# Performance work log

Measured on AMD Instinct MI355X. Metric: run time of the kernel, lower is better.

## Reference

```python
import jax, jax.numpy as jnp
import numpy as np

B, T, D = 4, 2048, 1024
H, KD, VD = 16, 64, 64  # num_heads, key_dim, value_dim; H*KD == D


def setup_inputs() -> dict:
    key = jax.random.key(0)
    ks = jax.random.split(key, 10)
    s = 0.02
    return {
        "q_in": jax.random.normal(ks[0], (B, T, D), jnp.float32),
        "v_in": jax.random.normal(ks[1], (B, T, D), jnp.float32),
        "Wq": jax.random.normal(ks[2], (D, H * KD), jnp.float32) * s,
        "bq": jnp.zeros((H * KD,), jnp.float32),
        "Wk": jax.random.normal(ks[3], (D, H * KD), jnp.float32) * s,
        "bk": jnp.zeros((H * KD,), jnp.float32),
        "Wv": jax.random.normal(ks[4], (D, H * VD), jnp.float32) * s,
        "bv": jnp.zeros((H * VD,), jnp.float32),
        "Wo": jax.random.normal(ks[5], (H * VD, D), jnp.float32) * s,
        "bo": jnp.zeros((D,), jnp.float32),
    }


def reference(q_in, v_in, Wq, bq, Wk, bk, Wv, bv, Wo, bo):
    # QKV projections (key defaults to value input)
    q = q_in @ Wq + bq                      # [B,T,H*KD]
    k = v_in @ Wk + bk                      # [B,T,H*KD]
    v = v_in @ Wv + bv                      # [B,T,H*VD]
    q = q.reshape(B, T, H, KD)
    k = k.reshape(B, T, H, KD)
    v = v.reshape(B, T, H, VD)
    # scaled dot-product attention, scores materialized as [B,H,Tq,Tv]
    q = q / jnp.sqrt(jnp.asarray(KD, q.dtype))
    scores = jnp.einsum('bqnh,bvnh->bnqv', q, k)
    weights = jax.nn.softmax(scores, axis=-1)
    out = jnp.einsum('bnqv,bvnh->bqnh', weights, v)  # [B,Tq,H,VD]
    out = out.reshape(B, T, H * VD)
    return out @ Wo + bo                    # [B,T,D]
```

## Files before the change

kernel.cpp:

```cpp
#include <hip/hip_runtime.h>

#define BATCH  4
#define T_SEQ  2048
#define NH     16
#define DMODEL 1024
#define HD     64

typedef float    f32x4 __attribute__((ext_vector_type(4)));
typedef _Float16 f16x8 __attribute__((ext_vector_type(8)));
typedef _Float16 f16x4 __attribute__((ext_vector_type(4)));
typedef __fp16   h16x2 __attribute__((ext_vector_type(2)));

#define LOG2E 1.44269504088896f

__device__ __forceinline__ void lds_load16(const void* g, void* l) {
  __builtin_amdgcn_global_load_lds((const __attribute__((address_space(1))) void*)g,
                                   (__attribute__((address_space(3))) void*)l, 16, 0, 0);
}

__device__ __forceinline__ f16x4 pack4_f16(float a, float b, float c, float d) {
  union { h16x2 h[2]; f16x4 f; } u;
  u.h[0] = __builtin_amdgcn_cvt_pkrtz(a, b);
  u.h[1] = __builtin_amdgcn_cvt_pkrtz(c, d);
  return u.f;
}

__global__ __launch_bounds__(256) void cast2_f32_to_f16(
    const float* __restrict__ a, const float* __restrict__ bsrc,
    _Float16* __restrict__ oa, _Float16* __restrict__ ob, int n4) {
  const float* in = blockIdx.y ? bsrc : a;
  _Float16* out = blockIdx.y ? ob : oa;
  int i = blockIdx.x * 256 + threadIdx.x;
  if (i < n4) {
    float4 v = ((const float4*)in)[i];
    f16x4 o = { (_Float16)v.x, (_Float16)v.y, (_Float16)v.z, (_Float16)v.w };
    ((f16x4*)out)[i] = o;
  }
}

__global__ __launch_bounds__(256) void transcast_w4(
    const float* __restrict__ W0, const float* __restrict__ W1,
    const float* __restrict__ W2, const float* __restrict__ W3,
    _Float16* __restrict__ T0, _Float16* __restrict__ T1,
    _Float16* __restrict__ T2, _Float16* __restrict__ T3) {
  const float* W; _Float16* Wt;
  switch (blockIdx.z) {
    case 0: W = W0; Wt = T0; break;
    case 1: W = W1; Wt = T1; break;
    case 2: W = W2; Wt = T2; break;
    default: W = W3; Wt = T3; break;
  }
  __shared__ float L[64][65];
  const int n0 = blockIdx.x * 64, k0 = blockIdx.y * 64;
  const int tx = threadIdx.x & 15, ty = threadIdx.x >> 4;
#pragma unroll
  for (int i = 0; i < 4; ++i) {
    float4 v = *(const float4*)&W[(size_t)(k0 + ty + 16 * i) * DMODEL + n0 + tx * 4];
    L[ty + 16 * i][tx * 4 + 0] = v.x;
    L[ty + 16 * i][tx * 4 + 1] = v.y;
    L[ty + 16 * i][tx * 4 + 2] = v.z;
    L[ty + 16 * i][tx * 4 + 3] = v.w;
  }
  __syncthreads();
#pragma unroll
  for (int i = 0; i < 4; ++i) {
    int n = n0 + ty + 16 * i;
    f16x4 o;
#pragma unroll
    for (int j = 0; j < 4; ++j) o[j] = (_Float16)L[tx * 4 + j][ty + 16 * i];
    *(f16x4*)&Wt[(size_t)n * DMODEL + k0 + tx * 4] = o;
  }
}

__device__ __forceinline__ void gemm2_body(
    const _Float16* __restrict__ A, const _Float16* __restrict__ Wt,
    const float* __restrict__ bias, void* __restrict__ Cout, float scale,
    int mode, _Float16* As0, _Float16* As1, _Float16* Bs0, _Float16* Bs1) {
  const int K = DMODEL;
  const int lane = threadIdx.x & 63, wave = threadIdx.x >> 6;
  const int bid = blockIdx.x + blockIdx.y * gridDim.x;
  const int m0 = ((bid & 7) * 4 + ((bid >> 3) & 3)) * 256;
  const int n0 = (bid >> 5) * 128;
  const int wm4 = (wave & 3) * 4;
  const int wn4 = (wave >> 2) * 4;
  const int m16 = lane & 15, quad = lane >> 4;

  const _Float16* ap[4]; const _Float16* bp[2];
#pragma unroll
  for (int j = 0; j < 4; ++j) {
    int g = wave * 4 + j;
    ap[j] = A + (size_t)(m0 + (g >> 1) * 16 + m16) * K + (g & 1) * 32 + quad * 8;
  }
#pragma unroll
  for (int j = 0; j < 2; ++j) {
    int g = wave * 2 + j;
    bp[j] = Wt + (size_t)(n0 + (g >> 1) * 16 + m16) * K + (g & 1) * 32 + quad * 8;
  }

  f32x4 acc[4][4] = {};

  _Float16 *Ac = As0, *An = As1, *Bc = Bs0, *Bn = Bs1;

#pragma unroll
  for (int j = 0; j < 4; ++j) lds_load16(ap[j], Ac + (wave * 4 + j) * 512);
#pragma unroll
  for (int j = 0; j < 2; ++j) lds_load16(bp[j], Bc + (wave * 2 + j) * 512);
  __syncthreads();

  for (int kt = 0; kt < 16; ++kt) {
    if (kt < 15) {
      const int k0 = (kt + 1) * 64;
#pragma unroll
      for (int j = 0; j < 4; ++j) lds_load16(ap[j] + k0, An + (wave * 4 + j) * 512);
#pragma unroll
      for (int j = 0; j < 2; ++j) lds_load16(bp[j] + k0, Bn + (wave * 2 + j) * 512);
    }
#pragma unroll
    for (int s = 0; s < 2; ++s) {
      f16x8 bf[4];
#pragma unroll
      for (int t = 0; t < 4; ++t)
        bf[t] = *(const f16x8*)(Bc + (((wn4 + t) * 2 + s) * 64 + lane) * 8);
#pragma unroll
      for (int mi = 0; mi < 4; ++mi) {
        f16x8 af = *(const f16x8*)(Ac + (((wm4 + mi) * 2 + s) * 64 + lane) * 8);
#pragma unroll
        for (int ni = 0; ni < 4; ++ni)
          acc[mi][ni] = __builtin_amdgcn_mfma_f32_16x16x32_f16(af, bf[ni], acc[mi][ni], 0, 0, 0);
      }
    }
    __syncthreads();
    _Float16* tA = Ac; Ac = An; An = tA;
    _Float16* tB = Bc; Bc = Bn; Bn = tB;
  }

  if (mode == 2) {
#pragma unroll
    for (int mi = 0; mi < 4; ++mi)
#pragma unroll
      for (int ni = 0; ni < 4; ++ni) {
        int row = m0 + (wm4 + mi) * 16 + quad * 4;
        int col = n0 + (wn4 + ni) * 16 + m16;
        int bb = row >> 11, tt = row & (T_SEQ - 1);
        int hh = col >> 6, dd = col & 63;
        float bv = bias[col];
        f16x4 pv = pack4_f16(acc[mi][ni][0] + bv, acc[mi][ni][1] + bv,
                             acc[mi][ni][2] + bv, acc[mi][ni][3] + bv);
        *(f16x4*)&((_Float16*)Cout)[(((size_t)bb * NH + hh) * HD + dd) * T_SEQ + tt] = pv;
      }
  } else if (mode == 0) {
#pragma unroll
    for (int mi = 0; mi < 4; ++mi)
#pragma unroll
      for (int r = 0; r < 4; ++r) {
        int row = m0 + (wm4 + mi) * 16 + quad * 4 + r;
#pragma unroll
        for (int ni = 0; ni < 4; ++ni) {
          int col = n0 + (wn4 + ni) * 16 + m16;
          float v = (acc[mi][ni][r] + bias[col]) * scale;
          ((_Float16*)Cout)[(size_t)row * DMODEL + col] = (_Float16)v;
        }
      }
  } else {
#pragma unroll
    for (int mi = 0; mi < 4; ++mi)
#pragma unroll
      for (int r = 0; r < 4; ++r) {
        int row = m0 + (wm4 + mi) * 16 + quad * 4 + r;
#pragma unroll
        for (int ni = 0; ni < 4; ++ni) {
          int col = n0 + (wn4 + ni) * 16 + m16;
          ((float*)Cout)[(size_t)row * DMODEL + col] = acc[mi][ni][r] + bias[col];
        }
      }
  }
}

__global__ __launch_bounds__(512, 2) void gemm_qkv(
    const _Float16* __restrict__ Aq, const _Float16* __restrict__ Av,
    const _Float16* __restrict__ Wq, const _Float16* __restrict__ Wk,
    const _Float16* __restrict__ Wv,
    const float* __restrict__ bq, const float* __restrict__ bk,
    const float* __restrict__ bv,
    _Float16* __restrict__ Cq, _Float16* __restrict__ Ck, _Float16* __restrict__ Cv) {
  __shared__ _Float16 As[2][256 * 64];
  __shared__ _Float16 Bs[2][128 * 64];
  const _Float16* A; const _Float16* Wt; const float* bias; _Float16* C;
  float scale; int mode;
  if (blockIdx.z == 0)      { A = Aq; Wt = Wq; bias = bq; C = Cq; scale = 0.125f * LOG2E; mode = 0; }
  else if (blockIdx.z == 1) { A = Av; Wt = Wk; bias = bk; C = Ck; scale = 1.f; mode = 0; }
  else                      { A = Av; Wt = Wv; bias = bv; C = Cv; scale = 1.f; mode = 2; }
  gemm2_body(A, Wt, bias, C, scale, mode, As[0], As[1], Bs[0], Bs[1]);
}

__global__ __launch_bounds__(512, 2) void gemm_out(
    const _Float16* __restrict__ A, const _Float16* __restrict__ Wt,
    const float* __restrict__ bias, float* __restrict__ Cout) {
  __shared__ _Float16 As[2][256 * 64];
  __shared__ _Float16 Bs[2][128 * 64];
  gemm2_body(A, Wt, bias, Cout, 1.f, 3, As[0], As[1], Bs[0], Bs[1]);
}

__global__ __launch_bounds__(256, 2) void attn_mfma(
    const _Float16* __restrict__ Q, const _Float16* __restrict__ Kb,
    const _Float16* __restrict__ Vt, _Float16* __restrict__ O) {
  __shared__ _Float16 Ks[64 * 64], Vs[64 * 64];
  __shared__ _Float16 Ps[4 * 4096];

  const int lane = threadIdx.x & 63, wave = threadIdx.x >> 6;
  const int m16 = lane & 15, quad = lane >> 4;
  const int h = blockIdx.x;
  const int q0 = blockIdx.y * 256;
  const int b = blockIdx.z;
  const int wq = wave * 64;
  const int wbase = wave * 4096;

  f16x8 qf[4][2];
#pragma unroll
  for (int mi = 0; mi < 4; ++mi)
#pragma unroll
    for (int ki = 0; ki < 2; ++ki) {
      int q = q0 + wq + mi * 16 + m16;
      qf[mi][ki] = *(const f16x8*)(Q + (((size_t)b * T_SEQ + q) * NH + h) * HD + ki * 32 + quad * 8);
    }

  const _Float16 *kp[2], *vp[2];
#pragma unroll
  for (int i = 0; i < 2; ++i) {
    int g = wave * 128 + i * 64 + lane;
    int tk = (g >> 7) * 16 + (g & 15);
    int dkof = ((g >> 6) & 1) * 32 + ((g >> 4) & 3) * 8;
    kp[i] = Kb + (((size_t)b * T_SEQ + tk) * NH + h) * HD + dkof;
    int dvof = (g >> 7) * 16 + (g & 15);
    int tv = ((g >> 6) & 1) * 32 + ((g >> 4) & 3) * 8;
    vp[i] = Vt + (((size_t)b * NH + h) * HD + dvof) * T_SEQ + tv;
  }

  int pw[4][4];
#pragma unroll
  for (int mi = 0; mi < 4; ++mi)
#pragma unroll
    for (int nt = 0; nt < 4; ++nt) {
      int kt = nt >> 1;
      int q8 = ((nt & 1) << 1) | (quad >> 1);
      pw[mi][nt] = wbase + ((mi * 2 + kt) * 64 + q8 * 16 + m16) * 8 + (quad & 1) * 4;
    }

  const f16x8 onef = {(_Float16)1, (_Float16)1, (_Float16)1, (_Float16)1,
                      (_Float16)1, (_Float16)1, (_Float16)1, (_Float16)1};

  f32x4 o_acc[4][4] = {};
  f32x4 l_acc[4] = {};

  for (int kv = 0; kv < T_SEQ; kv += 64) {
    __syncthreads();
#pragma unroll
    for (int i = 0; i < 2; ++i) {
      lds_load16(kp[i] + (size_t)kv * (NH * HD), Ks + (wave * 2 + i) * 512);
      lds_load16(vp[i] + kv, Vs + (wave * 2 + i) * 512);
    }
    __syncthreads();

    f32x4 st[4][4] = {};
#pragma unroll
    for (int nt = 0; nt < 4; ++nt)
#pragma unroll
      for (int ki = 0; ki < 2; ++ki) {
        f16x8 kf = *(const f16x8*)(Ks + ((nt * 2 + ki) * 64 + lane) * 8);
#pragma unroll
        for (int mi = 0; mi < 4; ++mi)
          st[mi][nt] = __builtin_amdgcn_mfma_f32_16x16x32_f16(kf, qf[mi][ki], st[mi][nt], 0, 0, 0);
      }

#pragma unroll
    for (int mi = 0; mi < 4; ++mi)
#pragma unroll
      for (int nt = 0; nt < 4; ++nt) {
        f16x4 p = pack4_f16(__builtin_amdgcn_exp2f(st[mi][nt][0]),
                            __builtin_amdgcn_exp2f(st[mi][nt][1]),
                            __builtin_amdgcn_exp2f(st[mi][nt][2]),
                            __builtin_amdgcn_exp2f(st[mi][nt][3]));
        *(f16x4*)(Ps + pw[mi][nt]) = p;
      }

#pragma unroll
    for (int kt = 0; kt < 2; ++kt) {
      f16x8 pf[4];
#pragma unroll
      for (int mi = 0; mi < 4; ++mi) {
        pf[mi] = *(const f16x8*)(Ps + wbase + ((mi * 2 + kt) * 64 + lane) * 8);
        l_acc[mi] = __builtin_amdgcn_mfma_f32_16x16x32_f16(pf[mi], onef, l_acc[mi], 0, 0, 0);
      }
#pragma unroll
      for (int nd = 0; nd < 4; ++nd) {
        f16x8 vf = *(const f16x8*)(Vs + ((nd * 2 + kt) * 64 + lane) * 8);
#pragma unroll
        for (int mi = 0; mi < 4; ++mi)
          o_acc[mi][nd] = __builtin_amdgcn_mfma_f32_16x16x32_f16(pf[mi], vf, o_acc[mi][nd], 0, 0, 0);
      }
    }
  }

#pragma unroll
  for (int mi = 0; mi < 4; ++mi)
#pragma unroll
    for (int r = 0; r < 4; ++r) {
      float inv = 1.f / l_acc[mi][r];
      int q = q0 + wq + mi * 16 + quad * 4 + r;
#pragma unroll
      for (int nd = 0; nd < 4; ++nd) {
        int d = nd * 16 + m16;
        O[(((size_t)b * T_SEQ + q) * NH + h) * HD + d] = (_Float16)(o_acc[mi][nd][r] * inv);
      }
    }
}

extern "C" void kernel_launch(void* const* d_in, const int* in_sizes, int n_in,
                              void* d_out, int out_size, void* d_ws, size_t ws_size,
                              hipStream_t stream) {
  const float* q_in = (const float*)d_in[0];
  const float* v_in = (const float*)d_in[1];
  const float* Wq   = (const float*)d_in[2];
  const float* bq   = (const float*)d_in[3];
  const float* Wk   = (const float*)d_in[4];
  const float* bk   = (const float*)d_in[5];
  const float* Wv   = (const float*)d_in[6];
  const float* bv   = (const float*)d_in[7];
  const float* Wo   = (const float*)d_in[8];
  const float* bo   = (const float*)d_in[9];
  float* out = (float*)d_out;

  const size_t MB = 1u << 20;
  char* ws = (char*)d_ws;
  _Float16* q16  = (_Float16*)(ws);
  _Float16* v16  = (_Float16*)(ws + 16 * MB);
  _Float16* qbuf = (_Float16*)(ws + 32 * MB);
  _Float16* kbuf = (_Float16*)(ws + 48 * MB);
  _Float16* vtb  = (_Float16*)(ws + 64 * MB);
  _Float16* Wqt  = (_Float16*)(ws + 80 * MB);
  _Float16* Wkt  = (_Float16*)(ws + 82 * MB);
  _Float16* Wvt  = (_Float16*)(ws + 84 * MB);
  _Float16* Wot  = (_Float16*)(ws + 86 * MB);

  const int n4 = BATCH * T_SEQ * DMODEL / 4;
  cast2_f32_to_f16<<<dim3(n4 / 256, 2), 256, 0, stream>>>(q_in, v_in, q16, v16, n4);

  transcast_w4<<<dim3(16, 16, 4), 256, 0, stream>>>(Wq, Wk, Wv, Wo, Wqt, Wkt, Wvt, Wot);

  gemm_qkv<<<dim3(8, 32, 3), 512, 0, stream>>>(q16, v16, Wqt, Wkt, Wvt, bq, bk, bv,
                                               qbuf, kbuf, vtb);

  attn_mfma<<<dim3(16, 8, 4), 256, 0, stream>>>(qbuf, kbuf, vtb, qbuf);

  gemm_out<<<dim3(8, 32), 512, 0, stream>>>(qbuf, Wot, bo, out);
}
```

Measured before the change: 345.8 us.

## Pipeline GEMM main loop at half-K-tile granularity with explicit vmcnt waits

Restructures the shared GEMM body so each 64-wide K tile is staged and consumed in two 32-wide halves. The next half is prefetched while the current one computes, and __syncthreads is replaced by s_waitcnt vmcnt(3) plus raw barriers. MFMA issue is wrapped in s_setprio, and fragment loads are hoisted ahead of the MFMA block. The aim is to overlap global-to-LDS copies with compute more finely and to cut barrier stalls. The hand-tuned waitcnt depends on the exact count of outstanding loads, which makes correctness fragile.

```diff
diff --git a/kernel.cpp b/kernel.cpp
--- a/kernel.cpp
+++ b/kernel.cpp
@@ -24,6 +24,10 @@
   u.h[1] = __builtin_amdgcn_cvt_pkrtz(c, d);
   return u.f;
 }
+
+#define MEMFENCE asm volatile("" ::: "memory")
+#define WAITVM3  asm volatile("s_waitcnt vmcnt(3)" ::: "memory")
+#define WAITVM0  asm volatile("s_waitcnt vmcnt(0)" ::: "memory")
 
 __global__ __launch_bounds__(256) void cast2_f32_to_f16(
     const float* __restrict__ a, const float* __restrict__ bsrc,
@@ -72,10 +76,10 @@
   }
 }
 
-__device__ __forceinline__ void gemm2_body(
+__device__ __forceinline__ void gemm8_body(
     const _Float16* __restrict__ A, const _Float16* __restrict__ Wt,
     const float* __restrict__ bias, void* __restrict__ Cout, float scale,
-    int mode, _Float16* As0, _Float16* As1, _Float16* Bs0, _Float16* Bs1) {
+    int mode, _Float16* As, _Float16* Bs) {
   const int K = DMODEL;
   const int lane = threadIdx.x & 63, wave = threadIdx.x >> 6;
   const int bid = blockIdx.x + blockIdx.y * gridDim.x;
@@ -85,54 +89,62 @@
   const int wn4 = (wave >> 2) * 4;
   const int m16 = lane & 15, quad = lane >> 4;
 
-  const _Float16* ap[4]; const _Float16* bp[2];
-#pragma unroll
-  for (int j = 0; j < 4; ++j) {
-    int g = wave * 4 + j;
-    ap[j] = A + (size_t)(m0 + (g >> 1) * 16 + m16) * K + (g & 1) * 32 + quad * 8;
-  }
-#pragma unroll
-  for (int j = 0; j < 2; ++j) {
-    int g = wave * 2 + j;
-    bp[j] = Wt + (size_t)(n0 + (g >> 1) * 16 + m16) * K + (g & 1) * 32 + quad * 8;
-  }
+  const _Float16* apg[2];
+  apg[0] = A + (size_t)(m0 + (wave * 2 + 0) * 16 + m16) * K + quad * 8;
+  apg[1] = A + (size_t)(m0 + (wave * 2 + 1) * 16 + m16) * K + quad * 8;
+  const _Float16* bpg = Wt + (size_t)(n0 + wave * 16 + m16) * K + quad * 8;
+
+  auto stage = [&](int buf, int s, int kofs) {
+    lds_load16(apg[0] + kofs, As + ((buf * 2 + s) * 16 + wave * 2 + 0) * 512);
+    lds_load16(apg[1] + kofs, As + ((buf * 2 + s) * 16 + wave * 2 + 1) * 512);
+    lds_load16(bpg + kofs,    Bs + ((buf * 2 + s) * 8 + wave) * 512);
+  };
 
   f32x4 acc[4][4] = {};
 
-  _Float16 *Ac = As0, *An = As1, *Bc = Bs0, *Bn = Bs1;
-
-#pragma unroll
-  for (int j = 0; j < 4; ++j) lds_load16(ap[j], Ac + (wave * 4 + j) * 512);
-#pragma unroll
-  for (int j = 0; j < 2; ++j) lds_load16(bp[j], Bc + (wave * 2 + j) * 512);
-  __syncthreads();
-
-  for (int kt = 0; kt < 16; ++kt) {
-    if (kt < 15) {
-      const int k0 = (kt + 1) * 64;
-#pragma unroll
-      for (int j = 0; j < 4; ++j) lds_load16(ap[j] + k0, An + (wave * 4 + j) * 512);
-#pragma unroll
-      for (int j = 0; j < 2; ++j) lds_load16(bp[j] + k0, Bn + (wave * 2 + j) * 512);
-    }
-#pragma unroll
-    for (int s = 0; s < 2; ++s) {
-      f16x8 bf[4];
-#pragma unroll
-      for (int t = 0; t < 4; ++t)
-        bf[t] = *(const f16x8*)(Bc + (((wn4 + t) * 2 + s) * 64 + lane) * 8);
-#pragma unroll
-      for (int mi = 0; mi < 4; ++mi) {
-        f16x8 af = *(const f16x8*)(Ac + (((wm4 + mi) * 2 + s) * 64 + lane) * 8);
-#pragma unroll
-        for (int ni = 0; ni < 4; ++ni)
-          acc[mi][ni] = __builtin_amdgcn_mfma_f32_16x16x32_f16(af, bf[ni], acc[mi][ni], 0, 0, 0);
-      }
-    }
-    __syncthreads();
-    _Float16* tA = Ac; Ac = An; An = tA;
-    _Float16* tB = Bc; Bc = Bn; Bn = tB;
-  }
+  auto compute = [&](int buf, int s) {
+    const _Float16* Ab = As + ((buf * 2 + s) * 16) * 512;
+    const _Float16* Bb = Bs + ((buf * 2 + s) * 8) * 512;
+    f16x8 af[4], bf[4];
+#pragma unroll
+    for (int ni = 0; ni < 4; ++ni)
+      bf[ni] = *(const f16x8*)(Bb + (wn4 + ni) * 512 + lane * 8);
+#pragma unroll
+    for (int mi = 0; mi < 4; ++mi)
+      af[mi] = *(const f16x8*)(Ab + (wm4 + mi) * 512 + lane * 8);
+    __builtin_amdgcn_s_setprio(1);
+#pragma unroll
+    for (int mi = 0; mi < 4; ++mi)
+#pragma unroll
+      for (int ni = 0; ni < 4; ++ni)
+        acc[mi][ni] = __builtin_amdgcn_mfma_f32_16x16x32_f16(af[mi], bf[ni], acc[mi][ni], 0, 0, 0);
+    __builtin_amdgcn_s_setprio(0);
+  };
+
+  stage(0, 0, 0);
+  stage(0, 1, 32);
+  WAITVM3;
+  __builtin_amdgcn_s_barrier();
+  MEMFENCE;
+
+  for (int t = 0; t < 15; ++t) {
+    const int buf = t & 1, nbuf = buf ^ 1;
+    stage(nbuf, 0, (t + 1) * 64);
+    compute(buf, 0);
+    WAITVM3;
+    __builtin_amdgcn_s_barrier();
+    MEMFENCE;
+    stage(nbuf, 1, (t + 1) * 64 + 32);
+    compute(buf, 1);
+    WAITVM3;
+    __builtin_amdgcn_s_barrier();
+    MEMFENCE;
+  }
+  compute(1, 0);
+  WAITVM0;
+  __builtin_amdgcn_s_barrier();
+  MEMFENCE;
+  compute(1, 1);
 
   if (mode == 2) {
 #pragma unroll
@@ -183,22 +195,22 @@
     const float* __restrict__ bq, const float* __restrict__ bk,
     const float* __restrict__ bv,
     _Float16* __restrict__ Cq, _Float16* __restrict__ Ck, _Float16* __restrict__ Cv) {
-  __shared__ _Float16 As[2][256 * 64];
-  __shared__ _Float16 Bs[2][128 * 64];
+  __shared__ _Float16 As[2 * 2 * 16 * 512];
+  __shared__ _Float16 Bs[2 * 2 * 8 * 512];
   const _Float16* A; const _Float16* Wt; const float* bias; _Float16* C;
   float scale; int mode;
   if (blockIdx.z == 0)      { A = Aq; Wt = Wq; bias = bq; C = Cq; scale = 0.125f * LOG2E; mode = 0; }
   else if (blockIdx.z == 1) { A = Av; Wt = Wk; bias = bk; C = Ck; scale = 1.f; mode = 0; }
   else                      { A = Av; Wt = Wv; bias = bv; C = Cv; scale = 1.f; mode = 2; }
-  gemm2_body(A, Wt, bias, C, scale, mode, As[0], As[1], Bs[0], Bs[1]);
+  gemm8_body(A, Wt, bias, C, scale, mode, As, Bs);
 }
 
 __global__ __launch_bounds__(512, 2) void gemm_out(
     const _Float16* __restrict__ A, const _Float16* __restrict__ Wt,
     const float* __restrict__ bias, float* __restrict__ Cout) {
-  __shared__ _Float16 As[2][256 * 64];
-  __shared__ _Float16 Bs[2][128 * 64];
-  gemm2_body(A, Wt, bias, Cout, 1.f, 3, As[0], As[1], Bs[0], Bs[1]);
+  __shared__ _Float16 As[2 * 2 * 16 * 512];
+  __shared__ _Float16 Bs[2 * 2 * 8 * 512];
+  gemm8_body(A, Wt, bias, Cout, 1.f, 3, As, Bs);
 }
 
 __global__ __launch_bounds__(256, 2) void attn_mfma(
```

Result: slower. 364.7 us (+5.5%).

## Shrink GEMM tiles to 128x128 with 256 threads and drop LDS double buffering

Applied to the files above, without the earlier changes.

Replaces the 256x128, 512-thread, double-buffered GEMM body with a 128x128 tile, 256-thread, single-buffered version that synchronises before and after each K-step load. The grid doubles along M and launch bounds allow three blocks per CU, trading reuse per tile and load/compute overlap for more blocks and less LDS per block. This may expose global-load latency, since the prefetch overlap is gone.

```diff
diff --git a/kernel.cpp b/kernel.cpp
--- a/kernel.cpp
+++ b/kernel.cpp
@@ -72,66 +72,51 @@
   }
 }
 
-__device__ __forceinline__ void gemm2_body(
+__device__ __forceinline__ void gemm97_body(
     const _Float16* __restrict__ A, const _Float16* __restrict__ Wt,
     const float* __restrict__ bias, void* __restrict__ Cout, float scale,
-    int mode, _Float16* As0, _Float16* As1, _Float16* Bs0, _Float16* Bs1) {
+    int mode, _Float16* As, _Float16* Bs) {
   const int K = DMODEL;
   const int lane = threadIdx.x & 63, wave = threadIdx.x >> 6;
   const int bid = blockIdx.x + blockIdx.y * gridDim.x;
-  const int m0 = ((bid & 7) * 4 + ((bid >> 3) & 3)) * 256;
-  const int n0 = (bid >> 5) * 128;
-  const int wm4 = (wave & 3) * 4;
-  const int wn4 = (wave >> 2) * 4;
+  const int m0 = ((bid & 7) * 8 + ((bid >> 3) & 7)) * 128;
+  const int n0 = (bid >> 6) * 128;
+  const int wr = (wave & 1) * 4;
+  const int wc = (wave >> 1) * 4;
   const int m16 = lane & 15, quad = lane >> 4;
 
-  const _Float16* ap[4]; const _Float16* bp[2];
+  const _Float16* ap[4]; const _Float16* bp[4];
 #pragma unroll
   for (int j = 0; j < 4; ++j) {
     int g = wave * 4 + j;
-    ap[j] = A + (size_t)(m0 + (g >> 1) * 16 + m16) * K + (g & 1) * 32 + quad * 8;
-  }
-#pragma unroll
-  for (int j = 0; j < 2; ++j) {
-    int g = wave * 2 + j;
+    ap[j] = A  + (size_t)(m0 + (g >> 1) * 16 + m16) * K + (g & 1) * 32 + quad * 8;
     bp[j] = Wt + (size_t)(n0 + (g >> 1) * 16 + m16) * K + (g & 1) * 32 + quad * 8;
   }
 
   f32x4 acc[4][4] = {};
 
-  _Float16 *Ac = As0, *An = As1, *Bc = Bs0, *Bn = Bs1;
-
-#pragma unroll
-  for (int j = 0; j < 4; ++j) lds_load16(ap[j], Ac + (wave * 4 + j) * 512);
-#pragma unroll
-  for (int j = 0; j < 2; ++j) lds_load16(bp[j], Bc + (wave * 2 + j) * 512);
-  __syncthreads();
-
-  for (int kt = 0; kt < 16; ++kt) {
-    if (kt < 15) {
-      const int k0 = (kt + 1) * 64;
-#pragma unroll
-      for (int j = 0; j < 4; ++j) lds_load16(ap[j] + k0, An + (wave * 4 + j) * 512);
-#pragma unroll
-      for (int j = 0; j < 2; ++j) lds_load16(bp[j] + k0, Bn + (wave * 2 + j) * 512);
-    }
+  for (int k0 = 0; k0 < 1024; k0 += 64) {
+    __syncthreads();
+#pragma unroll
+    for (int j = 0; j < 4; ++j) {
+      lds_load16(ap[j] + k0, As + (wave * 4 + j) * 512);
+      lds_load16(bp[j] + k0, Bs + (wave * 4 + j) * 512);
+    }
+    __syncthreads();
 #pragma unroll
     for (int s = 0; s < 2; ++s) {
       f16x8 bf[4];
 #pragma unroll
-      for (int t = 0; t < 4; ++t)
-        bf[t] = *(const f16x8*)(Bc + (((wn4 + t) * 2 + s) * 64 + lane) * 8);
+      for (int ni = 0; ni < 4; ++ni)
+        bf[ni] = *(const f16x8*)(Bs + (((wc + ni) * 2 + s) * 64 + lane) * 8);
 #pragma unroll
       for (int mi = 0; mi < 4; ++mi) {
-        f16x8 af = *(const f16x8*)(Ac + (((wm4 + mi) * 2 + s) * 64 + lane) * 8);
+        f16x8 af = *(const f16x8*)(As + (((wr + mi) * 2 + s) * 64 + lane) * 8);
 #pragma unroll
         for (int ni = 0; ni < 4; ++ni)
           acc[mi][ni] = __builtin_amdgcn_mfma_f32_16x16x32_f16(af, bf[ni], acc[mi][ni], 0, 0, 0);
       }
     }
-    __syncthreads();
-    _Float16* tA = Ac; Ac = An; An = tA;
-    _Float16* tB = Bc; Bc = Bn; Bn = tB;
   }
 
   if (mode == 2) {
@@ -139,8 +124,8 @@
     for (int mi = 0; mi < 4; ++mi)
 #pragma unroll
       for (int ni = 0; ni < 4; ++ni) {
-        int row = m0 + (wm4 + mi) * 16 + quad * 4;
-        int col = n0 + (wn4 + ni) * 16 + m16;
+        int row = m0 + (wr + mi) * 16 + quad * 4;
+        int col = n0 + (wc + ni) * 16 + m16;
         int bb = row >> 11, tt = row & (T_SEQ - 1);
         int hh = col >> 6, dd = col & 63;
         float bv = bias[col];
@@ -153,10 +138,10 @@
     for (int mi = 0; mi < 4; ++mi)
 #pragma unroll
       for (int r = 0; r < 4; ++r) {
-        int row = m0 + (wm4 + mi) * 16 + quad * 4 + r;
+        int row = m0 + (wr + mi) * 16 + quad * 4 + r;
 #pragma unroll
         for (int ni = 0; ni < 4; ++ni) {
-          int col = n0 + (wn4 + ni) * 16 + m16;
+          int col = n0 + (wc + ni) * 16 + m16;
           float v = (acc[mi][ni][r] + bias[col]) * scale;
           ((_Float16*)Cout)[(size_t)row * DMODEL + col] = (_Float16)v;
         }
@@ -166,39 +151,37 @@
     for (int mi = 0; mi < 4; ++mi)
 #pragma unroll
       for (int r = 0; r < 4; ++r) {
-        int row = m0 + (wm4 + mi) * 16 + quad * 4 + r;
+        int row = m0 + (wr + mi) * 16 + quad * 4 + r;
 #pragma unroll
         for (int ni = 0; ni < 4; ++ni) {
-          int col = n0 + (wn4 + ni) * 16 + m16;
+          int col = n0 + (wc + ni) * 16 + m16;
           ((float*)Cout)[(size_t)row * DMODEL + col] = acc[mi][ni][r] + bias[col];
         }
       }
   }
 }
 
-__global__ __launch_bounds__(512, 2) void gemm_qkv(
+__global__ __launch_bounds__(256, 3) void gemm_qkv(
     const _Float16* __restrict__ Aq, const _Float16* __restrict__ Av,
     const _Float16* __restrict__ Wq, const _Float16* __restrict__ Wk,
     const _Float16* __restrict__ Wv,
     const float* __restrict__ bq, const float* __restrict__ bk,
     const float* __restrict__ bv,
     _Float16* __restrict__ Cq, _Float16* __restrict__ Ck, _Float16* __restrict__ Cv) {
-  __shared__ _Float16 As[2][256 * 64];
-  __shared__ _Float16 Bs[2][128 * 64];
+  __shared__ _Float16 As[128 * 64], Bs[128 * 64];
   const _Float16* A; const _Float16* Wt; const float* bias; _Float16* C;
   float scale; int mode;
   if (blockIdx.z == 0)      { A = Aq; Wt = Wq; bias = bq; C = Cq; scale = 0.125f * LOG2E; mode = 0; }
   else if (blockIdx.z == 1) { A = Av; Wt = Wk; bias = bk; C = Ck; scale = 1.f; mode = 0; }
   else                      { A = Av; Wt = Wv; bias = bv; C = Cv; scale = 1.f; mode = 2; }
-  gemm2_body(A, Wt, bias, C, scale, mode, As[0], As[1], Bs[0], Bs[1]);
-}
-
-__global__ __launch_bounds__(512, 2) void gemm_out(
+  gemm97_body(A, Wt, bias, C, scale, mode, As, Bs);
+}
+
+__global__ __launch_bounds__(256, 3) void gemm_out(
     const _Float16* __restrict__ A, const _Float16* __restrict__ Wt,
     const float* __restrict__ bias, float* __restrict__ Cout) {
-  __shared__ _Float16 As[2][256 * 64];
-  __shared__ _Float16 Bs[2][128 * 64];
-  gemm2_body(A, Wt, bias, Cout, 1.f, 3, As[0], As[1], Bs[0], Bs[1]);
+  __shared__ _Float16 As[128 * 64], Bs[128 * 64];
+  gemm97_body(A, Wt, bias, Cout, 1.f, 3, As, Bs);
 }
 
 __global__ __launch_bounds__(256, 2) void attn_mfma(
@@ -347,10 +330,10 @@
 
   transcast_w4<<<dim3(16, 16, 4), 256, 0, stream>>>(Wq, Wk, Wv, Wo, Wqt, Wkt, Wvt, Wot);
 
-  gemm_qkv<<<dim3(8, 32, 3), 512, 0, stream>>>(q16, v16, Wqt, Wkt, Wvt, bq, bk, bv,
+  gemm_qkv<<<dim3(8, 64, 3), 256, 0, stream>>>(q16, v16, Wqt, Wkt, Wvt, bq, bk, bv,
                                                qbuf, kbuf, vtb);
 
   attn_mfma<<<dim3(16, 8, 4), 256, 0, stream>>>(qbuf, kbuf, vtb, qbuf);
 
-  gemm_out<<<dim3(8, 32), 512, 0, stream>>>(qbuf, Wot, bo, out);
-}
+  gemm_out<<<dim3(8, 64), 256, 0, stream>>>(qbuf, Wot, bo, out);
+}
```

Result: no change. 343.0 us (-0.8%).
